# Kernel optimization log

Measured on AMD Instinct MI355X. Metric: run time of the kernel, lower is better.

## Reference

```python
import jax, jax.numpy as jnp
import numpy as np

N_RAYS = 4096
NUM_STEPS = 768
MIN_NEAR_LIDAR = 0.01
LIDAR_MAX_DEPTH = 0.81
BOUND = 1.0
DENSITY_SCALE = 1.0
HID = 64
OUT_DIM = 2  # out_lidar_color_dim (intensity + raydrop)


def setup_inputs() -> dict:
    key = jax.random.key(0)
    ks = jax.random.split(key, 12)
    rays_o = jax.random.normal(ks[0], (N_RAYS, 3), jnp.float32) * 0.1
    rd = jax.random.normal(ks[1], (N_RAYS, 3), jnp.float32)
    rays_d = rd / jnp.linalg.norm(rd, axis=-1, keepdims=True)
    time = jax.random.uniform(ks[2], (N_RAYS, 1), jnp.float32)
    s = lambda fan: 1.0 / np.sqrt(fan)
    W1 = jax.random.normal(ks[3], (4, HID), jnp.float32) * s(4)
    b1 = jnp.zeros((HID,), jnp.float32)
    W2 = jax.random.normal(ks[4], (HID, HID), jnp.float32) * s(HID)
    b2 = jnp.zeros((HID,), jnp.float32)
    w_sig = jax.random.normal(ks[5], (HID, 1), jnp.float32) * s(HID)
    b_sig = jnp.zeros((1,), jnp.float32)
    Wc1 = jax.random.normal(ks[6], (3 + HID, HID), jnp.float32) * s(3 + HID)
    bc1 = jnp.zeros((HID,), jnp.float32)
    Wc2 = jax.random.normal(ks[7], (HID, OUT_DIM), jnp.float32) * s(HID)
    bc2 = jnp.zeros((OUT_DIM,), jnp.float32)
    return {"rays_o": rays_o, "rays_d": rays_d, "time": time,
            "W1": W1, "b1": b1, "W2": W2, "b2": b2,
            "w_sig": w_sig, "b_sig": b_sig,
            "Wc1": Wc1, "bc1": bc1, "Wc2": Wc2, "bc2": bc2}


def reference(rays_o, rays_d, time, W1, b1, W2, b2, w_sig, b_sig, Wc1, bc1, Wc2, bc2):
    N, S = rays_o.shape[0], NUM_STEPS
    nears = MIN_NEAR_LIDAR
    fars = LIDAR_MAX_DEPTH
    # stratified z values along each ray (no perturb)
    z = jnp.linspace(0.0, 1.0, S, dtype=rays_o.dtype)          # [S]
    z_vals = jnp.broadcast_to(nears + (fars - nears) * z, (N, S))
    sample_dist = (fars - nears) / S
    # sample points, clamped to AABB [-bound, bound]^3
    xyzs = rays_o[:, None, :] + rays_d[:, None, :] * z_vals[..., None]  # [N,S,3]
    xyzs = jnp.clip(xyzs, -BOUND, BOUND)
    # surrogate time-conditioned density field (NVSF 4D field)
    t = jnp.broadcast_to(time[:, None, :], (N, S, 1))
    h = jax.nn.relu(jnp.concatenate([xyzs, t], -1) @ W1 + b1)  # [N,S,HID]
    h = jax.nn.relu(h @ W2 + b2)
    sigma = jax.nn.softplus(h @ w_sig + b_sig)[..., 0]          # [N,S]
    # surrogate lidar color head (dir + geo features)
    dirs = jnp.broadcast_to(rays_d[:, None, :], (N, S, 3))
    c = jax.nn.relu(jnp.concatenate([dirs, h], -1) @ Wc1 + bc1)
    rgbs = jax.nn.sigmoid(c @ Wc2 + bc2)                        # [N,S,OUT_DIM]
    # alpha compositing
    deltas = z_vals[..., 1:] - z_vals[..., :-1]
    deltas = jnp.concatenate([deltas, jnp.full_like(deltas[..., :1], sample_dist)], -1)
    alphas = 1.0 - jnp.exp(-deltas * DENSITY_SCALE * sigma)     # [N,S]
    alphas_shifted = jnp.concatenate(
        [jnp.ones_like(alphas[..., :1]), 1.0 - alphas + 1e-15], -1)
    weights = alphas * jnp.cumprod(alphas_shifted, axis=-1)[..., :-1]
    weights_sum = jnp.sum(weights, axis=-1)                     # [N]
    depth = jnp.sum(weights * z_vals, axis=-1)                  # [N]
    image = jnp.sum(weights[..., None] * rgbs, axis=-2)         # [N,OUT_DIM]
    # lidar branch: no background compositing
    return depth, image, weights_sum, weights, z_vals
```

## Files before the change

kernel.cpp:

```cpp
#include <hip/hip_runtime.h>
#include <hip/hip_bf16.h>
#include <math.h>

#define NR 4096
#define NS 768

#define OFF_IMAGE   (NR)
#define OFF_WSUM    (NR*3)
#define OFF_WEIGHTS (NR*4)
#define OFF_ZVALS   (NR*4 + NR*NS)

typedef short bf16x8 __attribute__((ext_vector_type(8)));
typedef float f32x4  __attribute__((ext_vector_type(4)));

static __device__ __forceinline__ unsigned cvt_pk_bf16(float a, float b){
    unsigned r;
    asm("v_cvt_pk_bf16_f32 %0, %1, %2" : "=v"(r) : "v"(a), "v"(b));
    return r;
}
static __device__ __forceinline__ f32x4 zero4(){ f32x4 r = {0.f,0.f,0.f,0.f}; return r; }
static __device__ __forceinline__ void ldsfence(){ asm volatile("" ::: "memory"); }

__global__ __launch_bounds__(256, 2) void mlp_mfma_kernel(
    const float* __restrict__ rays_o, const float* __restrict__ rays_d,
    const float* __restrict__ timev,
    const float* __restrict__ W1, const float* __restrict__ b1,
    const float* __restrict__ W2, const float* __restrict__ b2,
    const float* __restrict__ w_sig, const float* __restrict__ b_sig,
    const float* __restrict__ Wc1, const float* __restrict__ bc1,
    const float* __restrict__ Wc2, const float* __restrict__ bc2,
    float* __restrict__ alpha_out,
    float* __restrict__ rgb_out)
{
    __shared__ __align__(16) unsigned bounce[4][2048];
    __shared__ __align__(16) unsigned stash[16*64*4];
    const int wid  = threadIdx.x >> 6;
    const int lane = threadIdx.x & 63;
    const int g = lane >> 4;
    const int c = lane & 15;

    if (wid == 0) {
        #pragma unroll
        for (int ft = 0; ft < 4; ++ft) {
            const int col = ft*16 + c;
            unsigned u0=0,u1=0,u2=0,u3=0, d0=0,d1=0;
            if (g == 0) {
                u0 = cvt_pk_bf16(W1[0*64+col], W1[1*64+col]);
                u1 = cvt_pk_bf16(W1[2*64+col], W1[3*64+col]);
                u2 = cvt_pk_bf16(b1[col], 0.f);
                d0 = cvt_pk_bf16(Wc1[0*64+col], Wc1[1*64+col]);
                d1 = cvt_pk_bf16(Wc1[2*64+col], bc1[col]);
            }
            unsigned* p = &stash[(ft*64 + lane)*4];
            p[0]=u0; p[1]=u1; p[2]=u2; p[3]=u3;
            unsigned* q = &stash[((4+ft)*64 + lane)*4];
            q[0]=d0; q[1]=d1; q[2]=0; q[3]=0;
        }
        #pragma unroll
        for (int kt = 0; kt < 2; ++kt) {
            unsigned s[4], w[4];
            #pragma unroll
            for (int p = 0; p < 4; ++p) {
                int k = kt*32 + 8*g + 2*p;
                s[p] = (c == 0) ? cvt_pk_bf16(w_sig[k], w_sig[k+1]) : 0u;
                w[p] = (c < 2)  ? cvt_pk_bf16(Wc2[k*2+c], Wc2[(k+1)*2+c]) : 0u;
            }
            unsigned* ps = &stash[((8+kt)*64 + lane)*4];
            ps[0]=s[0]; ps[1]=s[1]; ps[2]=s[2]; ps[3]=s[3];
            unsigned* pw = &stash[((10+kt)*64 + lane)*4];
            pw[0]=w[0]; pw[1]=w[1]; pw[2]=w[2]; pw[3]=w[3];
        }
        #pragma unroll
        for (int ft = 0; ft < 4; ++ft) {
            float* pb = reinterpret_cast<float*>(&stash[((12+ft)*64 + lane)*4]);
            #pragma unroll
            for (int r = 0; r < 4; ++r) pb[r] = b2[ft*16 + g*4 + r];
        }
    }

    auto ldfrag = [&](const float* __restrict__ W, int k0, int col)->bf16x8 {
        union { bf16x8 v; unsigned u[4]; } r;
        #pragma unroll
        for (int p = 0; p < 4; ++p) {
            int k = k0 + 2*p;
            r.u[p] = cvt_pk_bf16(W[k*64 + col], W[(k+1)*64 + col]);
        }
        return r.v;
    };
    bf16x8 bW2A[2][4], bWc1A[2][4];
    #pragma unroll
    for (int ft = 0; ft < 4; ++ft) {
        const int col = ft*16 + c;
        #pragma unroll
        for (int kt = 0; kt < 2; ++kt) {
            bW2A[kt][ft]  = ldfrag(W2,         kt*32 + 8*g, col);
            bWc1A[kt][ft] = ldfrag(Wc1 + 3*64, kt*32 + 8*g, col);
        }
    }
    const float bsg = b_sig[0];
    f32x4 bc2v;
    bc2v[0] = (g==0) ? bc2[0] : 0.f;
    bc2v[1] = (g==0) ? bc2[1] : 0.f;
    bc2v[2] = 0.f; bc2v[3] = 0.f;

    __syncthreads();

    unsigned* BW = &bounce[wid][0];
    const int wbase = (g>>1)*64 + c*4 + (g&1)*2;
    const int rbase = (g>>1)*128 + (g&1)*64 + c*4;
    auto SL = [&](int s)->bf16x8 {
        return *reinterpret_cast<const bf16x8*>(&stash[(s*64 + lane)*4]);
    };
    auto RD = [&](int kt, int nt)->bf16x8 {
        return *reinterpret_cast<const bf16x8*>(&BW[rbase + (nt*4 + kt*2)*128]);
    };

    const int gwave = blockIdx.x*4 + wid;

    #pragma unroll 1
    for (int tt = 0; tt < 6; ++tt) {
        const int tile = gwave*6 + tt;
        const int n  = tile / 12;
        const int s0 = (tile - n*12) * 64;
        const int s  = s0 + lane;

        const float z  = 0.01f + 0.8f * ((float)s * (1.0f/767.0f));
        const float ox = rays_o[3*n+0], oy = rays_o[3*n+1], oz = rays_o[3*n+2];
        const float dx = rays_d[3*n+0], dy = rays_d[3*n+1], dz = rays_d[3*n+2];
        const float tm = timev[n];

        const float px = fminf(fmaxf(fmaf(dx, z, ox), -1.f), 1.f);
        const float py = fminf(fmaxf(fmaf(dy, z, oy), -1.f), 1.f);
        const float pz = fminf(fmaxf(fmaf(dz, z, oz), -1.f), 1.f);
        const unsigned p01 = cvt_pk_bf16(px, py);
        const unsigned p23 = cvt_pk_bf16(pz, tm);

        f32x4 acc[4][4];

        {
            bf16x8 a1[4];
            #pragma unroll
            for (int ft = 0; ft < 4; ++ft) a1[ft] = SL(ft);
            #pragma unroll
            for (int nt = 0; nt < 4; ++nt) {
                unsigned q0 = (unsigned)__shfl((int)p01, nt*16 + c);
                unsigned q1 = (unsigned)__shfl((int)p23, nt*16 + c);
                union { bf16x8 v; unsigned u[4]; } b;
                b.u[0] = (g==0) ? q0 : 0u;
                b.u[1] = (g==0) ? q1 : 0u;
                b.u[2] = (g==0) ? 0x00003F80u : 0u;
                b.u[3] = 0u;
                #pragma unroll
                for (int ft = 0; ft < 4; ++ft)
                    acc[ft][nt] = __builtin_amdgcn_mfma_f32_16x16x32_bf16(
                        a1[ft], b.v, zero4(), 0, 0, 0);
            }
        }
        ldsfence();
        #pragma unroll
        for (int ft = 0; ft < 4; ++ft)
            #pragma unroll
            for (int nt = 0; nt < 4; ++nt) {
                unsigned pk0 = cvt_pk_bf16(fmaxf(acc[ft][nt][0],0.f), fmaxf(acc[ft][nt][1],0.f));
                unsigned pk1 = cvt_pk_bf16(fmaxf(acc[ft][nt][2],0.f), fmaxf(acc[ft][nt][3],0.f));
                *reinterpret_cast<uint2*>(&BW[wbase + (nt*4+ft)*128]) = make_uint2(pk0, pk1);
            }
        ldsfence();

        {
            f32x4 b2v[4];
            #pragma unroll
            for (int ft = 0; ft < 4; ++ft)
                b2v[ft] = *reinterpret_cast<const f32x4*>(&stash[((12+ft)*64 + lane)*4]);
            #pragma unroll
            for (int nt = 0; nt < 4; ++nt) {
                bf16x8 f0 = RD(0, nt), f1 = RD(1, nt);
                #pragma unroll
                for (int ft = 0; ft < 4; ++ft) {
                    f32x4 d = __builtin_amdgcn_mfma_f32_16x16x32_bf16(bW2A[0][ft], f0, b2v[ft], 0,0,0);
                    acc[ft][nt] = __builtin_amdgcn_mfma_f32_16x16x32_bf16(bW2A[1][ft], f1, d, 0,0,0);
                }
            }
        }
        ldsfence();
        #pragma unroll
        for (int ft = 0; ft < 4; ++ft)
            #pragma unroll
            for (int nt = 0; nt < 4; ++nt) {
                unsigned pk0 = cvt_pk_bf16(fmaxf(acc[ft][nt][0],0.f), fmaxf(acc[ft][nt][1],0.f));
                unsigned pk1 = cvt_pk_bf16(fmaxf(acc[ft][nt][2],0.f), fmaxf(acc[ft][nt][3],0.f));
                *reinterpret_cast<uint2*>(&BW[wbase + (nt*4+ft)*128]) = make_uint2(pk0, pk1);
            }
        ldsfence();

        f32x4 sigD[4];
        {
            bf16x8 ad[4];
            #pragma unroll
            for (int ft = 0; ft < 4; ++ft) ad[ft] = SL(4+ft);
            bf16x8 ws0 = SL(8), ws1 = SL(9);
            union { bf16x8 v; unsigned u[4]; } fd;
            fd.u[0] = (g==0) ? cvt_pk_bf16(dx, dy) : 0u;
            fd.u[1] = (g==0) ? cvt_pk_bf16(dz, 1.0f) : 0u;
            fd.u[2] = 0u; fd.u[3] = 0u;
            #pragma unroll
            for (int nt = 0; nt < 4; ++nt) {
                bf16x8 f0 = RD(0, nt), f1 = RD(1, nt);
                #pragma unroll
                for (int ft = 0; ft < 4; ++ft) {
                    f32x4 d = __builtin_amdgcn_mfma_f32_16x16x32_bf16(bWc1A[0][ft], f0, zero4(), 0,0,0);
                    d = __builtin_amdgcn_mfma_f32_16x16x32_bf16(bWc1A[1][ft], f1, d, 0,0,0);
                    acc[ft][nt] = __builtin_amdgcn_mfma_f32_16x16x32_bf16(ad[ft], fd.v, d, 0,0,0);
                }
                f32x4 sd = __builtin_amdgcn_mfma_f32_16x16x32_bf16(ws0, f0, zero4(), 0,0,0);
                sigD[nt] = __builtin_amdgcn_mfma_f32_16x16x32_bf16(ws1, f1, sd, 0,0,0);
            }
        }
        ldsfence();
        #pragma unroll
        for (int ft = 0; ft < 4; ++ft)
            #pragma unroll
            for (int nt = 0; nt < 4; ++nt) {
                unsigned pk0 = cvt_pk_bf16(fmaxf(acc[ft][nt][0],0.f), fmaxf(acc[ft][nt][1],0.f));
                unsigned pk1 = cvt_pk_bf16(fmaxf(acc[ft][nt][2],0.f), fmaxf(acc[ft][nt][3],0.f));
                *reinterpret_cast<uint2*>(&BW[wbase + (nt*4+ft)*128]) = make_uint2(pk0, pk1);
            }
        ldsfence();

        {
            float v0 = __shfl(sigD[0][0], c);
            float v1 = __shfl(sigD[1][0], c);
            float v2 = __shfl(sigD[2][0], c);
            float v3 = __shfl(sigD[3][0], c);
            float pre = (g==0) ? v0 : ((g==1) ? v1 : ((g==2) ? v2 : v3));
            pre += bsg;
            float sig = fmaxf(pre, 0.f) + __logf(1.f + __expf(-fabsf(pre)));
            float dl  = (s == NS-1) ? (0.8f/768.0f) : (0.8f/767.0f);
            alpha_out[tile*64 + lane] = 1.0f - __expf(-dl * sig);
        }

        {
            bf16x8 c20 = SL(10), c21 = SL(11);
            f32x4 rgbD[4];
            #pragma unroll
            for (int nt = 0; nt < 4; ++nt) {
                bf16x8 f0 = RD(0, nt), f1 = RD(1, nt);
                f32x4 d = __builtin_amdgcn_mfma_f32_16x16x32_bf16(c20, f0, bc2v, 0,0,0);
                rgbD[nt] = __builtin_amdgcn_mfma_f32_16x16x32_bf16(c21, f1, d, 0,0,0);
            }
            ldsfence();
            float a0 = __shfl(rgbD[0][0], c), b0 = __shfl(rgbD[0][1], c);
            float a1 = __shfl(rgbD[1][0], c), b1v_ = __shfl(rgbD[1][1], c);
            float a2 = __shfl(rgbD[2][0], c), b2_ = __shfl(rgbD[2][1], c);
            float a3 = __shfl(rgbD[3][0], c), b3 = __shfl(rgbD[3][1], c);
            float r0 = (g==0) ? a0 : ((g==1) ? a1 : ((g==2) ? a2 : a3));
            float r1 = (g==0) ? b0 : ((g==1) ? b1v_ : ((g==2) ? b2_ : b3));
            r0 = 1.0f / (1.0f + __expf(-r0));
            r1 = 1.0f / (1.0f + __expf(-r1));
            *reinterpret_cast<float2*>(&rgb_out[2*(tile*64 + lane)]) = make_float2(r0, r1);
        }
    }
}

__global__ __launch_bounds__(256) void composite_kernel(
    const float* __restrict__ rgb,
    float* __restrict__ out)
{
    int gtid = blockIdx.x * 256 + threadIdx.x;
    int ray  = gtid >> 6;
    int lane = threadIdx.x & 63;
    if (ray >= NR) return;

    float* __restrict__ depth_o = out;
    float* __restrict__ image_o = out + OFF_IMAGE;
    float* __restrict__ wsum_o  = out + OFF_WSUM;
    float* __restrict__ w_o     = out + OFF_WEIGHTS;
    float* __restrict__ z_o     = out + OFF_ZVALS;

    float T = 1.0f;
    float depth = 0.0f, wsum = 0.0f, im0 = 0.0f, im1 = 0.0f;

    for (int ch = 0; ch < NS/64; ++ch) {
        int s   = ch*64 + lane;
        int idx = ray*NS + s;
        float a  = w_o[idx];
        float zv = 0.01f + 0.8f * ((float)s * (1.0f/767.0f));
        float f  = 1.0f - a + 1e-15f;

        float p = f;
        #pragma unroll
        for (int off = 1; off < 64; off <<= 1) {
            float v = __shfl_up(p, off, 64);
            if (lane >= off) p *= v;
        }
        float excl = __shfl_up(p, 1, 64);
        if (lane == 0) excl = 1.0f;

        float wgt = a * T * excl;

        float r0 = rgb[2*idx + 0], r1 = rgb[2*idx + 1];
        depth = fmaf(wgt, zv, depth);
        wsum += wgt;
        im0   = fmaf(wgt, r0, im0);
        im1   = fmaf(wgt, r1, im1);

        w_o[idx] = wgt;
        z_o[idx] = zv;

        T *= __shfl(p, 63, 64);
    }

    #pragma unroll
    for (int off = 32; off >= 1; off >>= 1) {
        depth += __shfl_down(depth, off, 64);
        wsum  += __shfl_down(wsum , off, 64);
        im0   += __shfl_down(im0  , off, 64);
        im1   += __shfl_down(im1  , off, 64);
    }
    if (lane == 0) {
        depth_o[ray]      = depth;
        image_o[2*ray+0]  = im0;
        image_o[2*ray+1]  = im1;
        wsum_o[ray]       = wsum;
    }
}

extern "C" void kernel_launch(void* const* d_in, const int* in_sizes, int n_in,
                              void* d_out, int out_size, void* d_ws, size_t ws_size,
                              hipStream_t stream) {
    const float* rays_o = (const float*)d_in[0];
    const float* rays_d = (const float*)d_in[1];
    const float* timev  = (const float*)d_in[2];
    const float* W1     = (const float*)d_in[3];
    const float* b1     = (const float*)d_in[4];
    const float* W2     = (const float*)d_in[5];
    const float* b2     = (const float*)d_in[6];
    const float* w_sig  = (const float*)d_in[7];
    const float* b_sig  = (const float*)d_in[8];
    const float* Wc1    = (const float*)d_in[9];
    const float* bc1    = (const float*)d_in[10];
    const float* Wc2    = (const float*)d_in[11];
    const float* bc2    = (const float*)d_in[12];

    float* out   = (float*)d_out;
    float* alpha = out + OFF_WEIGHTS;
    float* rgb   = (float*)d_ws;

    dim3 blk(256);
    hipLaunchKernelGGL(mlp_mfma_kernel, dim3(2048), blk, 0, stream,
                       rays_o, rays_d, timev, W1, b1, W2, b2, w_sig, b_sig,
                       Wc1, bc1, Wc2, bc2, alpha, rgb);

    hipLaunchKernelGGL(composite_kernel, dim3((NR*64)/256), blk, 0, stream, rgb, out);
}
```

Measured before the change: 112.1 us.

## Process two sample tiles per wave iteration to interleave MFMA chains

Each wave now handles two 64-sample tiles per loop iteration. The tiles use separate LDS bounce buffers and separate accumulator sets, so the independent MFMA chains and LDS round-trips of both tiles can overlap and hide latency. In exchange the per-wave LDS footprint doubles and accumulator register pressure roughly doubles. That may cause spills or lower occupancy under launch_bounds(256,2).

New measurement: 120.0 us. 1.07x slower.

```diff
diff --git a/kernel.cpp b/kernel.cpp
--- a/kernel.cpp
+++ b/kernel.cpp
@@ -32,7 +32,7 @@
     float* __restrict__ alpha_out,
     float* __restrict__ rgb_out)
 {
-    __shared__ __align__(16) unsigned bounce[4][2048];
+    __shared__ __align__(16) unsigned bounce[4][4096];
     __shared__ __align__(16) unsigned stash[16*64*4];
     const int wid  = threadIdx.x >> 6;
     const int lane = threadIdx.x & 63;
@@ -105,37 +105,53 @@
 
     __syncthreads();
 
-    unsigned* BW = &bounce[wid][0];
+    unsigned* BWA = &bounce[wid][0];
+    unsigned* BWB = &bounce[wid][2048];
     const int wbase = (g>>1)*64 + c*4 + (g&1)*2;
     const int rbase = (g>>1)*128 + (g&1)*64 + c*4;
     auto SL = [&](int s)->bf16x8 {
         return *reinterpret_cast<const bf16x8*>(&stash[(s*64 + lane)*4]);
     };
-    auto RD = [&](int kt, int nt)->bf16x8 {
+    auto RDp = [&](unsigned* BW, int kt, int nt)->bf16x8 {
         return *reinterpret_cast<const bf16x8*>(&BW[rbase + (nt*4 + kt*2)*128]);
     };
+    auto WRp = [&](unsigned* BW, const f32x4& a, int F){
+        unsigned pk0 = cvt_pk_bf16(fmaxf(a[0],0.f), fmaxf(a[1],0.f));
+        unsigned pk1 = cvt_pk_bf16(fmaxf(a[2],0.f), fmaxf(a[3],0.f));
+        *reinterpret_cast<uint2*>(&BW[wbase + F*128]) = make_uint2(pk0, pk1);
+    };
 
     const int gwave = blockIdx.x*4 + wid;
 
     #pragma unroll 1
-    for (int tt = 0; tt < 6; ++tt) {
-        const int tile = gwave*6 + tt;
-        const int n  = tile / 12;
-        const int s0 = (tile - n*12) * 64;
-        const int s  = s0 + lane;
-
-        const float z  = 0.01f + 0.8f * ((float)s * (1.0f/767.0f));
-        const float ox = rays_o[3*n+0], oy = rays_o[3*n+1], oz = rays_o[3*n+2];
-        const float dx = rays_d[3*n+0], dy = rays_d[3*n+1], dz = rays_d[3*n+2];
-        const float tm = timev[n];
-
-        const float px = fminf(fmaxf(fmaf(dx, z, ox), -1.f), 1.f);
-        const float py = fminf(fmaxf(fmaf(dy, z, oy), -1.f), 1.f);
-        const float pz = fminf(fmaxf(fmaf(dz, z, oz), -1.f), 1.f);
-        const unsigned p01 = cvt_pk_bf16(px, py);
-        const unsigned p23 = cvt_pk_bf16(pz, tm);
-
-        f32x4 acc[4][4];
+    for (int tp = 0; tp < 3; ++tp) {
+        const int tileA = gwave*6 + tp*2;
+        const int tileB = tileA + 1;
+
+        const int nA = tileA / 12, nB = tileB / 12;
+        const int sA = (tileA - nA*12)*64 + lane;
+        const int sB = (tileB - nB*12)*64 + lane;
+        const float zA = 0.01f + 0.8f * ((float)sA * (1.0f/767.0f));
+        const float zB = 0.01f + 0.8f * ((float)sB * (1.0f/767.0f));
+        const float oxA = rays_o[3*nA+0], oyA = rays_o[3*nA+1], ozA = rays_o[3*nA+2];
+        const float dxA = rays_d[3*nA+0], dyA = rays_d[3*nA+1], dzA = rays_d[3*nA+2];
+        const float tmA = timev[nA];
+        const float oxB = rays_o[3*nB+0], oyB = rays_o[3*nB+1], ozB = rays_o[3*nB+2];
+        const float dxB = rays_d[3*nB+0], dyB = rays_d[3*nB+1], dzB = rays_d[3*nB+2];
+        const float tmB = timev[nB];
+
+        const unsigned p01A = cvt_pk_bf16(
+            fminf(fmaxf(fmaf(dxA, zA, oxA), -1.f), 1.f),
+            fminf(fmaxf(fmaf(dyA, zA, oyA), -1.f), 1.f));
+        const unsigned p23A = cvt_pk_bf16(
+            fminf(fmaxf(fmaf(dzA, zA, ozA), -1.f), 1.f), tmA);
+        const unsigned p01B = cvt_pk_bf16(
+            fminf(fmaxf(fmaf(dxB, zB, oxB), -1.f), 1.f),
+            fminf(fmaxf(fmaf(dyB, zB, oyB), -1.f), 1.f));
+        const unsigned p23B = cvt_pk_bf16(
+            fminf(fmaxf(fmaf(dzB, zB, ozB), -1.f), 1.f), tmB);
+
+        f32x4 accA[4][4], accB[4][4];
 
         {
             bf16x8 a1[4];
@@ -143,8 +159,8 @@
             for (int ft = 0; ft < 4; ++ft) a1[ft] = SL(ft);
             #pragma unroll
             for (int nt = 0; nt < 4; ++nt) {
-                unsigned q0 = (unsigned)__shfl((int)p01, nt*16 + c);
-                unsigned q1 = (unsigned)__shfl((int)p23, nt*16 + c);
+                unsigned q0 = (unsigned)__shfl((int)p01A, nt*16 + c);
+                unsigned q1 = (unsigned)__shfl((int)p23A, nt*16 + c);
                 union { bf16x8 v; unsigned u[4]; } b;
                 b.u[0] = (g==0) ? q0 : 0u;
                 b.u[1] = (g==0) ? q1 : 0u;
@@ -152,19 +168,33 @@
                 b.u[3] = 0u;
                 #pragma unroll
                 for (int ft = 0; ft < 4; ++ft)
-                    acc[ft][nt] = __builtin_amdgcn_mfma_f32_16x16x32_bf16(
+                    accA[ft][nt] = __builtin_amdgcn_mfma_f32_16x16x32_bf16(
                         a1[ft], b.v, zero4(), 0, 0, 0);
             }
-        }
-        ldsfence();
-        #pragma unroll
-        for (int ft = 0; ft < 4; ++ft)
-            #pragma unroll
-            for (int nt = 0; nt < 4; ++nt) {
-                unsigned pk0 = cvt_pk_bf16(fmaxf(acc[ft][nt][0],0.f), fmaxf(acc[ft][nt][1],0.f));
-                unsigned pk1 = cvt_pk_bf16(fmaxf(acc[ft][nt][2],0.f), fmaxf(acc[ft][nt][3],0.f));
-                *reinterpret_cast<uint2*>(&BW[wbase + (nt*4+ft)*128]) = make_uint2(pk0, pk1);
-            }
+            #pragma unroll
+            for (int nt = 0; nt < 4; ++nt) {
+                unsigned q0 = (unsigned)__shfl((int)p01B, nt*16 + c);
+                unsigned q1 = (unsigned)__shfl((int)p23B, nt*16 + c);
+                union { bf16x8 v; unsigned u[4]; } b;
+                b.u[0] = (g==0) ? q0 : 0u;
+                b.u[1] = (g==0) ? q1 : 0u;
+                b.u[2] = (g==0) ? 0x00003F80u : 0u;
+                b.u[3] = 0u;
+                #pragma unroll
+                for (int ft = 0; ft < 4; ++ft)
+                    accB[ft][nt] = __builtin_amdgcn_mfma_f32_16x16x32_bf16(
+                        a1[ft], b.v, zero4(), 0, 0, 0);
+            }
+        }
+        ldsfence();
+        #pragma unroll
+        for (int ft = 0; ft < 4; ++ft)
+            #pragma unroll
+            for (int nt = 0; nt < 4; ++nt) { WRp(BWA, accA[ft][nt], nt*4+ft); }
+        #pragma unroll
+        for (int ft = 0; ft < 4; ++ft)
+            #pragma unroll
+            for (int nt = 0; nt < 4; ++nt) { WRp(BWB, accB[ft][nt], nt*4+ft); }
         ldsfence();
 
         {
@@ -174,90 +204,144 @@
                 b2v[ft] = *reinterpret_cast<const f32x4*>(&stash[((12+ft)*64 + lane)*4]);
             #pragma unroll
             for (int nt = 0; nt < 4; ++nt) {
-                bf16x8 f0 = RD(0, nt), f1 = RD(1, nt);
+                bf16x8 f0 = RDp(BWA, 0, nt), f1 = RDp(BWA, 1, nt);
                 #pragma unroll
                 for (int ft = 0; ft < 4; ++ft) {
                     f32x4 d = __builtin_amdgcn_mfma_f32_16x16x32_bf16(bW2A[0][ft], f0, b2v[ft], 0,0,0);
-                    acc[ft][nt] = __builtin_amdgcn_mfma_f32_16x16x32_bf16(bW2A[1][ft], f1, d, 0,0,0);
+                    accA[ft][nt] = __builtin_amdgcn_mfma_f32_16x16x32_bf16(bW2A[1][ft], f1, d, 0,0,0);
                 }
             }
-        }
-        ldsfence();
-        #pragma unroll
-        for (int ft = 0; ft < 4; ++ft)
-            #pragma unroll
-            for (int nt = 0; nt < 4; ++nt) {
-                unsigned pk0 = cvt_pk_bf16(fmaxf(acc[ft][nt][0],0.f), fmaxf(acc[ft][nt][1],0.f));
-                unsigned pk1 = cvt_pk_bf16(fmaxf(acc[ft][nt][2],0.f), fmaxf(acc[ft][nt][3],0.f));
-                *reinterpret_cast<uint2*>(&BW[wbase + (nt*4+ft)*128]) = make_uint2(pk0, pk1);
-            }
-        ldsfence();
-
-        f32x4 sigD[4];
+            #pragma unroll
+            for (int nt = 0; nt < 4; ++nt) {
+                bf16x8 f0 = RDp(BWB, 0, nt), f1 = RDp(BWB, 1, nt);
+                #pragma unroll
+                for (int ft = 0; ft < 4; ++ft) {
+                    f32x4 d = __builtin_amdgcn_mfma_f32_16x16x32_bf16(bW2A[0][ft], f0, b2v[ft], 0,0,0);
+                    accB[ft][nt] = __builtin_amdgcn_mfma_f32_16x16x32_bf16(bW2A[1][ft], f1, d, 0,0,0);
+                }
+            }
+        }
+        ldsfence();
+        #pragma unroll
+        for (int ft = 0; ft < 4; ++ft)
+            #pragma unroll
+            for (int nt = 0; nt < 4; ++nt) { WRp(BWA, accA[ft][nt], nt*4+ft); }
+        #pragma unroll
+        for (int ft = 0; ft < 4; ++ft)
+            #pragma unroll
+            for (int nt = 0; nt < 4; ++nt) { WRp(BWB, accB[ft][nt], nt*4+ft); }
+        ldsfence();
+
+        f32x4 sigDA[4], sigDB[4];
         {
             bf16x8 ad[4];
             #pragma unroll
             for (int ft = 0; ft < 4; ++ft) ad[ft] = SL(4+ft);
             bf16x8 ws0 = SL(8), ws1 = SL(9);
-            union { bf16x8 v; unsigned u[4]; } fd;
-            fd.u[0] = (g==0) ? cvt_pk_bf16(dx, dy) : 0u;
-            fd.u[1] = (g==0) ? cvt_pk_bf16(dz, 1.0f) : 0u;
-            fd.u[2] = 0u; fd.u[3] = 0u;
-            #pragma unroll
-            for (int nt = 0; nt < 4; ++nt) {
-                bf16x8 f0 = RD(0, nt), f1 = RD(1, nt);
+            union { bf16x8 v; unsigned u[4]; } fdA, fdB;
+            fdA.u[0] = (g==0) ? cvt_pk_bf16(dxA, dyA) : 0u;
+            fdA.u[1] = (g==0) ? cvt_pk_bf16(dzA, 1.0f) : 0u;
+            fdA.u[2] = 0u; fdA.u[3] = 0u;
+            fdB.u[0] = (g==0) ? cvt_pk_bf16(dxB, dyB) : 0u;
+            fdB.u[1] = (g==0) ? cvt_pk_bf16(dzB, 1.0f) : 0u;
+            fdB.u[2] = 0u; fdB.u[3] = 0u;
+            #pragma unroll
+            for (int nt = 0; nt < 4; ++nt) {
+                bf16x8 f0 = RDp(BWA, 0, nt), f1 = RDp(BWA, 1, nt);
                 #pragma unroll
                 for (int ft = 0; ft < 4; ++ft) {
                     f32x4 d = __builtin_amdgcn_mfma_f32_16x16x32_bf16(bWc1A[0][ft], f0, zero4(), 0,0,0);
                     d = __builtin_amdgcn_mfma_f32_16x16x32_bf16(bWc1A[1][ft], f1, d, 0,0,0);
-                    acc[ft][nt] = __builtin_amdgcn_mfma_f32_16x16x32_bf16(ad[ft], fd.v, d, 0,0,0);
+                    accA[ft][nt] = __builtin_amdgcn_mfma_f32_16x16x32_bf16(ad[ft], fdA.v, d, 0,0,0);
                 }
                 f32x4 sd = __builtin_amdgcn_mfma_f32_16x16x32_bf16(ws0, f0, zero4(), 0,0,0);
-                sigD[nt] = __builtin_amdgcn_mfma_f32_16x16x32_bf16(ws1, f1, sd, 0,0,0);
-            }
-        }
-        ldsfence();
-        #pragma unroll
-        for (int ft = 0; ft < 4; ++ft)
-            #pragma unroll
-            for (int nt = 0; nt < 4; ++nt) {
-                unsigned pk0 = cvt_pk_bf16(fmaxf(acc[ft][nt][0],0.f), fmaxf(acc[ft][nt][1],0.f));
-                unsigned pk1 = cvt_pk_bf16(fmaxf(acc[ft][nt][2],0.f), fmaxf(acc[ft][nt][3],0.f));
-                *reinterpret_cast<uint2*>(&BW[wbase + (nt*4+ft)*128]) = make_uint2(pk0, pk1);
-            }
-        ldsfence();
-
-        {
-            float v0 = __shfl(sigD[0][0], c);
-            float v1 = __shfl(sigD[1][0], c);
-            float v2 = __shfl(sigD[2][0], c);
-            float v3 = __shfl(sigD[3][0], c);
+                sigDA[nt] = __builtin_amdgcn_mfma_f32_16x16x32_bf16(ws1, f1, sd, 0,0,0);
+            }
+            #pragma unroll
+            for (int nt = 0; nt < 4; ++nt) {
+                bf16x8 f0 = RDp(BWB, 0, nt), f1 = RDp(BWB, 1, nt);
+                #pragma unroll
+                for (int ft = 0; ft < 4; ++ft) {
+                    f32x4 d = __builtin_amdgcn_mfma_f32_16x16x32_bf16(bWc1A[0][ft], f0, zero4(), 0,0,0);
+                    d = __builtin_amdgcn_mfma_f32_16x16x32_bf16(bWc1A[1][ft], f1, d, 0,0,0);
+                    accB[ft][nt] = __builtin_amdgcn_mfma_f32_16x16x32_bf16(ad[ft], fdB.v, d, 0,0,0);
+                }
+                f32x4 sd = __builtin_amdgcn_mfma_f32_16x16x32_bf16(ws0, f0, zero4(), 0,0,0);
+                sigDB[nt] = __builtin_amdgcn_mfma_f32_16x16x32_bf16(ws1, f1, sd, 0,0,0);
+            }
+        }
+        ldsfence();
+        #pragma unroll
+        for (int ft = 0; ft < 4; ++ft)
+            #pragma unroll
+            for (int nt = 0; nt < 4; ++nt) { WRp(BWA, accA[ft][nt], nt*4+ft); }
+        #pragma unroll
+        for (int ft = 0; ft < 4; ++ft)
+            #pragma unroll
+            for (int nt = 0; nt < 4; ++nt) { WRp(BWB, accB[ft][nt], nt*4+ft); }
+        ldsfence();
+
+        {
+            float v0 = __shfl(sigDA[0][0], c);
+            float v1 = __shfl(sigDA[1][0], c);
+            float v2 = __shfl(sigDA[2][0], c);
+            float v3 = __shfl(sigDA[3][0], c);
             float pre = (g==0) ? v0 : ((g==1) ? v1 : ((g==2) ? v2 : v3));
             pre += bsg;
             float sig = fmaxf(pre, 0.f) + __logf(1.f + __expf(-fabsf(pre)));
-            float dl  = (s == NS-1) ? (0.8f/768.0f) : (0.8f/767.0f);
-            alpha_out[tile*64 + lane] = 1.0f - __expf(-dl * sig);
+            float dl  = (sA == NS-1) ? (0.8f/768.0f) : (0.8f/767.0f);
+            alpha_out[tileA*64 + lane] = 1.0f - __expf(-dl * sig);
+        }
+        {
+            float v0 = __shfl(sigDB[0][0], c);
+            float v1 = __shfl(sigDB[1][0], c);
+            float v2 = __shfl(sigDB[2][0], c);
+            float v3 = __shfl(sigDB[3][0], c);
+            float pre = (g==0) ? v0 : ((g==1) ? v1 : ((g==2) ? v2 : v3));
+            pre += bsg;
+            float sig = fmaxf(pre, 0.f) + __logf(1.f + __expf(-fabsf(pre)));
+            float dl  = (sB == NS-1) ? (0.8f/768.0f) : (0.8f/767.0f);
+            alpha_out[tileB*64 + lane] = 1.0f - __expf(-dl * sig);
         }
 
         {
             bf16x8 c20 = SL(10), c21 = SL(11);
-            f32x4 rgbD[4];
-            #pragma unroll
-            for (int nt = 0; nt < 4; ++nt) {
-                bf16x8 f0 = RD(0, nt), f1 = RD(1, nt);
+            f32x4 rgbDA[4], rgbDB[4];
+            #pragma unroll
+            for (int nt = 0; nt < 4; ++nt) {
+                bf16x8 f0 = RDp(BWA, 0, nt), f1 = RDp(BWA, 1, nt);
                 f32x4 d = __builtin_amdgcn_mfma_f32_16x16x32_bf16(c20, f0, bc2v, 0,0,0);
-                rgbD[nt] = __builtin_amdgcn_mfma_f32_16x16x32_bf16(c21, f1, d, 0,0,0);
+                rgbDA[nt] = __builtin_amdgcn_mfma_f32_16x16x32_bf16(c21, f1, d, 0,0,0);
+            }
+            #pragma unroll
+            for (int nt = 0; nt < 4; ++nt) {
+                bf16x8 f0 = RDp(BWB, 0, nt), f1 = RDp(BWB, 1, nt);
+                f32x4 d = __builtin_amdgcn_mfma_f32_16x16x32_bf16(c20, f0, bc2v, 0,0,0);
+                rgbDB[nt] = __builtin_amdgcn_mfma_f32_16x16x32_bf16(c21, f1, d, 0,0,0);
             }
             ldsfence();
-            float a0 = __shfl(rgbD[0][0], c), b0 = __shfl(rgbD[0][1], c);
-            float a1 = __shfl(rgbD[1][0], c), b1v_ = __shfl(rgbD[1][1], c);
-            float a2 = __shfl(rgbD[2][0], c), b2_ = __shfl(rgbD[2][1], c);
-            float a3 = __shfl(rgbD[3][0], c), b3 = __shfl(rgbD[3][1], c);
-            float r0 = (g==0) ? a0 : ((g==1) ? a1 : ((g==2) ? a2 : a3));
-            float r1 = (g==0) ? b0 : ((g==1) ? b1v_ : ((g==2) ? b2_ : b3));
-            r0 = 1.0f / (1.0f + __expf(-r0));
-            r1 = 1.0f / (1.0f + __expf(-r1));
-            *reinterpret_cast<float2*>(&rgb_out[2*(tile*64 + lane)]) = make_float2(r0, r1);
+            {
+                float a0 = __shfl(rgbDA[0][0], c), b0 = __shfl(rgbDA[0][1], c);
+                float a1 = __shfl(rgbDA[1][0], c), b1v_ = __shfl(rgbDA[1][1], c);
+                float a2 = __shfl(rgbDA[2][0], c), b2_ = __shfl(rgbDA[2][1], c);
+                float a3 = __shfl(rgbDA[3][0], c), b3 = __shfl(rgbDA[3][1], c);
+                float r0 = (g==0) ? a0 : ((g==1) ? a1 : ((g==2) ? a2 : a3));
+                float r1 = (g==0) ? b0 : ((g==1) ? b1v_ : ((g==2) ? b2_ : b3));
+                r0 = 1.0f / (1.0f + __expf(-r0));
+                r1 = 1.0f / (1.0f + __expf(-r1));
+                *reinterpret_cast<float2*>(&rgb_out[2*(tileA*64 + lane)]) = make_float2(r0, r1);
+            }
+            {
+                float a0 = __shfl(rgbDB[0][0], c), b0 = __shfl(rgbDB[0][1], c);
+                float a1 = __shfl(rgbDB[1][0], c), b1v_ = __shfl(rgbDB[1][1], c);
+                float a2 = __shfl(rgbDB[2][0], c), b2_ = __shfl(rgbDB[2][1], c);
+                float a3 = __shfl(rgbDB[3][0], c), b3 = __shfl(rgbDB[3][1], c);
+                float r0 = (g==0) ? a0 : ((g==1) ? a1 : ((g==2) ? a2 : a3));
+                float r1 = (g==0) ? b0 : ((g==1) ? b1v_ : ((g==2) ? b2_ : b3));
+                r0 = 1.0f / (1.0f + __expf(-r0));
+                r1 = 1.0f / (1.0f + __expf(-r1));
+                *reinterpret_cast<float2*>(&rgb_out[2*(tileB*64 + lane)]) = make_float2(r0, r1);
+            }
         }
     }
 }
```
